# Optimization experiments

Measured on AMD Instinct MI355X. Metric: run time of the kernel, lower is better.

## Reference

```python
import jax, jax.numpy as jnp
import numpy as np

N_NODES = 100000
N_EDGES = 600000
D_IN = 128
D_OUT = 128
N_REL = 16
N_BASES = 8


def setup_inputs() -> dict:
    key = jax.random.key(0)
    ks = jax.random.split(key, 6)
    x = jax.random.normal(ks[0], (N_NODES, D_IN), dtype=jnp.float32)
    edge_index = jax.random.randint(ks[1], (2, N_EDGES), 0, N_NODES, dtype=jnp.int64)
    edge_type = jax.random.randint(ks[2], (N_EDGES,), 0, N_REL, dtype=jnp.int64)
    # xavier-uniform-ish init scales
    b_lim = float(np.sqrt(6.0 / (D_IN + D_OUT)))
    c_lim = float(np.sqrt(6.0 / (N_REL + N_BASES)))
    w_lim = float(np.sqrt(6.0 / (D_IN + D_OUT)))
    bases = jax.random.uniform(ks[3], (N_BASES, D_IN, D_OUT), jnp.float32, -b_lim, b_lim)
    coefficients = jax.random.uniform(ks[4], (N_REL, N_BASES), jnp.float32, -c_lim, c_lim)
    w_self = jax.random.uniform(ks[5], (D_OUT, D_IN), jnp.float32, -w_lim, w_lim)
    return {"x": x, "edge_index": edge_index, "edge_type": edge_type,
            "bases": bases, "coefficients": coefficients, "w_self": w_self}


def reference(x, edge_index, edge_type, bases, coefficients, w_self):
    # self loop: Linear(in, out, bias=False) -> x @ W^T
    out = x @ w_self.T  # [N, D_OUT]
    # relation weights from basis decomposition
    weights = jnp.einsum('rb,bio->rio', coefficients, bases)  # [R, D_IN, D_OUT]
    row, col = edge_index[0], edge_index[1]
    xc = x[col]  # [E, D_IN] gather of source features
    n_rel = weights.shape[0]
    msg = jnp.zeros((xc.shape[0], w_self.shape[0]), dtype=x.dtype)
    # fixed small loop over relations; masked accumulate matches per-relation grouped GEMM
    for r in range(n_rel):
        sel = (edge_type == r)[:, None]
        msg = msg + jnp.where(sel, xc @ weights[r], jnp.zeros((), x.dtype))
    # scatter-add messages to destination rows
    out = out.at[row].add(msg)
    return out
```

## Files before the change

kernel.cpp:

```cpp
#include <hip/hip_runtime.h>

#define NN 100000
#define NE 600000
#define ET (NE + NN)
#define D 128
#define NREL 16
#define SCANB 391

typedef short short8 __attribute__((ext_vector_type(8)));
typedef float f32x4 __attribute__((ext_vector_type(4)));

#define C0 0
#define O0 20
#define CU0 40
#define T0 60

#define WT_OFF 0
#define META_OFF 557056
#define DH_OFF   557568
#define DO_OFF   957568
#define DC_OFF   1357576
#define BS_OFF   1757576
#define SC_OFF   1759168
#define SR_OFF   4559168
#define MP_OFF   7359168
#define MSG_OFF  10159168
#define NEED_A   (MSG_OFF + (size_t)ET * 128 * 2)

__device__ __forceinline__ unsigned short f2bf(float f) {
  unsigned u = __builtin_bit_cast(unsigned, f);
  u += 0x7fffu + ((u >> 16) & 1u);
  return (unsigned short)(u >> 16);
}

__global__ __launch_bounds__(256) void k_weights(const float* __restrict__ bases,
    const float* __restrict__ coef, const float* __restrict__ w_self,
    unsigned short* __restrict__ wT)
{
  int idx = blockIdx.x * 256 + threadIdx.x;
  int r = idx >> 14;
  int t = idx & 16383;
  float v;
  if (r < 16) {
    int o = t >> 7, i = t & 127;
    float acc = 0.f;
    #pragma unroll
    for (int b = 0; b < 8; ++b)
      acc += coef[r * 8 + b] * bases[b * 16384 + i * 128 + o];
    v = acc;
  } else {
    v = w_self[t];
  }
  wT[idx] = f2bf(v);
}

__global__ __launch_bounds__(256) void k_hist(const int* __restrict__ ei,
    const int* __restrict__ et, int* __restrict__ meta, int* __restrict__ dstHist)
{
  __shared__ int h[16];
  int tid = threadIdx.x;
  if (tid < 16) h[tid] = 0;
  __syncthreads();
  for (int e = blockIdx.x * 256 + tid; e < NE; e += gridDim.x * 256) {
    atomicAdd(&h[et[e]], 1);
    atomicAdd(&dstHist[ei[e]], 1);
  }
  __syncthreads();
  if (tid < 16) atomicAdd(&meta[C0 + tid], h[tid]);
}

__global__ __launch_bounds__(256) void k_scan1(const int* __restrict__ dstHist,
    int* __restrict__ dstOff, int* __restrict__ blockSums)
{
  __shared__ int sh[256];
  int tid = threadIdx.x;
  int d = blockIdx.x * 256 + tid;
  int v = (d < NN) ? (dstHist[d] + 1) : 0;
  sh[tid] = v;
  __syncthreads();
  #pragma unroll
  for (int ofs = 1; ofs < 256; ofs <<= 1) {
    int t = (tid >= ofs) ? sh[tid - ofs] : 0;
    __syncthreads();
    sh[tid] += t;
    __syncthreads();
  }
  if (d < NN) dstOff[d] = sh[tid] - v;
  if (tid == 255) blockSums[blockIdx.x] = sh[tid];
}

__global__ __launch_bounds__(512) void k_scan2(int* __restrict__ blockSums, int* __restrict__ meta)
{
  __shared__ int sh[SCANB];
  int tid = threadIdx.x;
  if (tid < SCANB) sh[tid] = blockSums[tid];
  __syncthreads();
  if (tid == 0) {
    int run = 0;
    for (int i = 0; i < SCANB; ++i) { int c = sh[i]; sh[i] = run; run += c; }
    meta[C0 + 16] = NN;
    int off = 0, toff = 0;
    for (int r = 0; r <= 16; ++r) {
      meta[O0 + r] = off;
      meta[CU0 + r] = off;
      meta[T0 + r] = toff;
      int c = meta[C0 + r];
      off += c;
      toff += (c + 63) >> 6;
    }
    meta[O0 + 17] = off;
    meta[T0 + 17] = toff;
  }
  __syncthreads();
  if (tid < SCANB) blockSums[tid] = sh[tid];
}

__global__ __launch_bounds__(256) void k_scan3(int* __restrict__ dstOff,
    const int* __restrict__ blockSums, int* __restrict__ dstCursor)
{
  int tid = threadIdx.x;
  int d = blockIdx.x * 256 + tid;
  int base = blockSums[blockIdx.x];
  if (d < NN) {
    int o = dstOff[d] + base;
    dstOff[d] = o;
    dstCursor[d] = o;
  }
  if (d == NN) dstOff[NN] = ET;
}

__global__ __launch_bounds__(256) void k_self(int* __restrict__ sCol, int* __restrict__ sRow,
    int* __restrict__ mpos, int* __restrict__ dstCursor, int doMsg)
{
  int n = blockIdx.x * 256 + threadIdx.x;
  if (n < NN) {
    sCol[NE + n] = n;
    sRow[NE + n] = n;
    if (doMsg) mpos[NE + n] = atomicAdd(&dstCursor[n], 1);
  }
}

__global__ __launch_bounds__(256) void k_scatter(const int* __restrict__ ei, const int* __restrict__ et,
    int* __restrict__ meta, int* __restrict__ sCol, int* __restrict__ sRow,
    int* __restrict__ mpos, int* __restrict__ dstCursor, int doMsg)
{
  __shared__ int h[16], base[16], lh[16];
  int tid = threadIdx.x;
  int start = blockIdx.x * 4096;
  int end = min(NE, start + 4096);
  if (tid < 16) { h[tid] = 0; lh[tid] = 0; }
  __syncthreads();
  for (int e = start + tid; e < end; e += 256)
    atomicAdd(&h[et[e]], 1);
  __syncthreads();
  if (tid < 16) base[tid] = atomicAdd(&meta[CU0 + tid], h[tid]);
  __syncthreads();
  for (int e = start + tid; e < end; e += 256) {
    int r = et[e];
    int row = ei[e];
    int pos = base[r] + atomicAdd(&lh[r], 1);
    sCol[pos] = ei[NE + e];
    sRow[pos] = row;
    if (doMsg) mpos[pos] = atomicAdd(&dstCursor[row], 1);
  }
}

__global__ __launch_bounds__(256) void k_gemm(const float* __restrict__ x,
    const unsigned short* __restrict__ wT, const int* __restrict__ meta,
    const int* __restrict__ sCol, const int* __restrict__ sRow,
    const int* __restrict__ mpos, unsigned short* __restrict__ msg,
    float* __restrict__ out, int mode)
{
  __shared__ short As[64 * 17 * 8];
  __shared__ int Rows[64];
  __shared__ int Pos[64];
  int b = blockIdx.x;
  if (b >= meta[T0 + 17]) return;
  int r = 0;
  while (r < 16 && meta[T0 + r + 1] <= b) ++r;
  int tile = b - meta[T0 + r];
  int boff = meta[O0 + r];
  int bcnt = meta[C0 + r];
  int e0 = boff + tile * 64;
  int nrows = min(64, boff + bcnt - e0);

  int tid = threadIdx.x;
  int lane = tid & 63, wave = tid >> 6;
  int q = lane >> 4, l15 = lane & 15;

  const unsigned short* wr = wT + r * 16384;
  short8 bf[2][4];
  #pragma unroll
  for (int ns = 0; ns < 2; ++ns) {
    #pragma unroll
    for (int kk = 0; kk < 4; ++kk) {
      int n = wave * 32 + ns * 16 + l15;
      bf[ns][kk] = *(const short8*)(wr + n * 128 + kk * 32 + q * 8);
    }
  }

  int m = tid >> 2, ug = tid & 3;
  bool valid = m < nrows;
  int c = valid ? sCol[e0 + m] : 0;
  const float* xr = x + c * 128;
  #pragma unroll
  for (int s = 0; s < 4; ++s) {
    int u = ug * 4 + s;
    float4 f0 = make_float4(0.f, 0.f, 0.f, 0.f), f1 = f0;
    if (valid) {
      f0 = *(const float4*)(xr + u * 8);
      f1 = *(const float4*)(xr + u * 8 + 4);
    }
    short8 pk;
    pk[0] = (short)f2bf(f0.x); pk[1] = (short)f2bf(f0.y);
    pk[2] = (short)f2bf(f0.z); pk[3] = (short)f2bf(f0.w);
    pk[4] = (short)f2bf(f1.x); pk[5] = (short)f2bf(f1.y);
    pk[6] = (short)f2bf(f1.z); pk[7] = (short)f2bf(f1.w);
    *(short8*)&As[(m * 17 + u) * 8] = pk;
  }
  if (tid < 64) {
    Rows[tid] = (tid < nrows) ? sRow[e0 + tid] : 0;
    Pos[tid] = (mode && tid < nrows) ? mpos[e0 + tid] : 0;
  }
  __syncthreads();

  f32x4 acc[4][2];
  #pragma unroll
  for (int ms = 0; ms < 4; ++ms)
    #pragma unroll
    for (int ns = 0; ns < 2; ++ns)
      acc[ms][ns] = (f32x4){0.f, 0.f, 0.f, 0.f};

  #pragma unroll
  for (int kk = 0; kk < 4; ++kk) {
    short8 af[4];
    #pragma unroll
    for (int ms = 0; ms < 4; ++ms)
      af[ms] = *(const short8*)&As[((ms * 16 + l15) * 17 + kk * 4 + q) * 8];
    #pragma unroll
    for (int ms = 0; ms < 4; ++ms)
      #pragma unroll
      for (int ns = 0; ns < 2; ++ns)
        acc[ms][ns] = __builtin_amdgcn_mfma_f32_16x16x32_bf16(af[ms], bf[ns][kk], acc[ms][ns], 0, 0, 0);
  }

  if (mode) {
    #pragma unroll
    for (int ms = 0; ms < 4; ++ms) {
      #pragma unroll
      for (int reg = 0; reg < 4; ++reg) {
        int mrow = ms * 16 + q * 4 + reg;
        if (mrow < nrows) {
          unsigned short* mp = msg + (size_t)Pos[mrow] * 128 + wave * 32 + l15;
          mp[0]  = f2bf(acc[ms][0][reg]);
          mp[16] = f2bf(acc[ms][1][reg]);
        }
      }
    }
  } else {
    #pragma unroll
    for (int ms = 0; ms < 4; ++ms) {
      #pragma unroll
      for (int reg = 0; reg < 4; ++reg) {
        int mrow = ms * 16 + q * 4 + reg;
        if (mrow < nrows) {
          float* op = out + (size_t)Rows[mrow] * 128 + wave * 32 + l15;
          unsafeAtomicAdd(op, acc[ms][0][reg]);
          unsafeAtomicAdd(op + 16, acc[ms][1][reg]);
        }
      }
    }
  }
}

__global__ __launch_bounds__(256) void k_reduce(const unsigned short* __restrict__ msg,
    const int* __restrict__ dstOff, float* __restrict__ out)
{
  int d = blockIdx.x * 4 + (threadIdx.x >> 6);
  if (d >= NN) return;
  int lane = threadIdx.x & 63;
  int s = dstOff[d], e = dstOff[d + 1];
  float a0 = 0.f, a1 = 0.f;
  const unsigned int* base = (const unsigned int*)msg;
  for (int j = s; j < e; ++j) {
    unsigned int v = base[(size_t)j * 64 + lane];
    a0 += __builtin_bit_cast(float, v << 16);
    a1 += __builtin_bit_cast(float, v & 0xffff0000u);
  }
  float2 w; w.x = a0; w.y = a1;
  *(float2*)(out + (size_t)d * 128 + lane * 2) = w;
}

extern "C" void kernel_launch(void* const* d_in, const int* in_sizes, int n_in,
                              void* d_out, int out_size, void* d_ws, size_t ws_size,
                              hipStream_t stream)
{
  const float* x      = (const float*)d_in[0];
  const int*   ei     = (const int*)d_in[1];
  const int*   et     = (const int*)d_in[2];
  const float* bases  = (const float*)d_in[3];
  const float* coef   = (const float*)d_in[4];
  const float* w_self = (const float*)d_in[5];
  float* out = (float*)d_out;
  char* ws = (char*)d_ws;
  unsigned short* wT = (unsigned short*)(ws + WT_OFF);
  int* meta      = (int*)(ws + META_OFF);
  int* dstHist   = (int*)(ws + DH_OFF);
  int* dstOff    = (int*)(ws + DO_OFF);
  int* dstCursor = (int*)(ws + DC_OFF);
  int* blockSums = (int*)(ws + BS_OFF);
  int* sCol      = (int*)(ws + SC_OFF);
  int* sRow      = (int*)(ws + SR_OFF);
  int* mpos      = (int*)(ws + MP_OFF);
  unsigned short* msg = (unsigned short*)(ws + MSG_OFF);

  const int modeA = (ws_size >= NEED_A) ? 1 : 0;

  hipMemsetAsync(ws + META_OFF, 0, 512 + 400000, stream);
  k_weights<<<(17 * 16384) / 256, 256, 0, stream>>>(bases, coef, w_self, wT);
  k_hist<<<256, 256, 0, stream>>>(ei, et, meta, dstHist);
  if (modeA) {
    k_scan1<<<SCANB, 256, 0, stream>>>(dstHist, dstOff, blockSums);
    k_scan2<<<1, 512, 0, stream>>>(blockSums, meta);
    k_scan3<<<SCANB, 256, 0, stream>>>(dstOff, blockSums, dstCursor);
  } else {
    k_scan2<<<1, 512, 0, stream>>>(blockSums, meta);
    hipMemsetAsync(d_out, 0, (size_t)NN * D * 4, stream);
  }
  k_self<<<SCANB, 256, 0, stream>>>(sCol, sRow, mpos, dstCursor, modeA);
  k_scatter<<<(NE + 4095) / 4096, 256, 0, stream>>>(ei, et, meta, sCol, sRow, mpos, dstCursor, modeA);
  k_gemm<<<10954, 256, 0, stream>>>(x, wT, meta, sCol, sRow, mpos, msg, out, modeA);
  if (modeA)
    k_reduce<<<(NN + 3) / 4, 256, 0, stream>>>(msg, dstOff, out);
}
```

Before: 396.4 us.

## Precast x to bf16, fold self-loop setup into scan, use nontemporal msg traffic

Adds a pre-pass that converts x to bf16 once, so the GEMM gathers half as many bytes per edge row and skips per-tile conversion, at the cost of an extra full pass over x and more workspace. The self-loop index setup moves into k_scan3, which assigns each self-loop the first slot of its destination segment directly instead of using an atomic, and one launch is removed. Message stores and reduce loads become nontemporal, and the reduce loop is unrolled by two with split accumulators for more memory-level parallelism. The bf16 path only runs when the workspace is large enough.

After: 391.5 us. Within noise of the previous version (-1.2%).

```diff
diff --git a/kernel.cpp b/kernel.cpp
--- a/kernel.cpp
+++ b/kernel.cpp
@@ -20,12 +20,15 @@
 #define DH_OFF   557568
 #define DO_OFF   957568
 #define DC_OFF   1357576
-#define BS_OFF   1757576
-#define SC_OFF   1759168
-#define SR_OFF   4559168
-#define MP_OFF   7359168
-#define MSG_OFF  10159168
-#define NEED_A   (MSG_OFF + (size_t)ET * 128 * 2)
+#define BS_OFF   1759168
+#define SC_OFF   1761168
+#define SR_OFF   4561168
+#define MP_OFF   7361168
+#define XB_OFF   10161168
+#define MSGB_OFF 35761168
+#define MSGA_OFF 10161168
+#define NEED_B   (MSGB_OFF + (size_t)ET * 128 * 2)
+#define NEED_A   (MSGA_OFF + (size_t)ET * 128 * 2)
 
 __device__ __forceinline__ unsigned short f2bf(float f) {
   unsigned u = __builtin_bit_cast(unsigned, f);
@@ -52,6 +55,20 @@
     v = w_self[t];
   }
   wT[idx] = f2bf(v);
+}
+
+__global__ __launch_bounds__(256) void k_xcast(const float* __restrict__ x,
+    unsigned short* __restrict__ xb)
+{
+  int i = blockIdx.x * 256 + threadIdx.x;
+  if (i >= NN * D / 4) return;
+  float4 f = *(const float4*)(x + (size_t)i * 4);
+  short8 dummy;
+  unsigned short s0 = f2bf(f.x), s1 = f2bf(f.y), s2 = f2bf(f.z), s3 = f2bf(f.w);
+  (void)dummy;
+  unsigned long long pk = (unsigned long long)s0 | ((unsigned long long)s1 << 16)
+                        | ((unsigned long long)s2 << 32) | ((unsigned long long)s3 << 48);
+  *(unsigned long long*)(xb + (size_t)i * 4) = pk;
 }
 
 __global__ __launch_bounds__(256) void k_hist(const int* __restrict__ ei,
@@ -116,7 +133,8 @@
 }
 
 __global__ __launch_bounds__(256) void k_scan3(int* __restrict__ dstOff,
-    const int* __restrict__ blockSums, int* __restrict__ dstCursor)
+    const int* __restrict__ blockSums, int* __restrict__ dstCursor,
+    int* __restrict__ sCol, int* __restrict__ sRow, int* __restrict__ mpos)
 {
   int tid = threadIdx.x;
   int d = blockIdx.x * 256 + tid;
@@ -124,20 +142,18 @@
   if (d < NN) {
     int o = dstOff[d] + base;
     dstOff[d] = o;
-    dstCursor[d] = o;
+    dstCursor[d] = o + 1;
+    sCol[NE + d] = d;
+    sRow[NE + d] = d;
+    mpos[NE + d] = o;
   }
   if (d == NN) dstOff[NN] = ET;
 }
 
-__global__ __launch_bounds__(256) void k_self(int* __restrict__ sCol, int* __restrict__ sRow,
-    int* __restrict__ mpos, int* __restrict__ dstCursor, int doMsg)
+__global__ __launch_bounds__(256) void k_self0(int* __restrict__ sCol, int* __restrict__ sRow)
 {
   int n = blockIdx.x * 256 + threadIdx.x;
-  if (n < NN) {
-    sCol[NE + n] = n;
-    sRow[NE + n] = n;
-    if (doMsg) mpos[NE + n] = atomicAdd(&dstCursor[n], 1);
-  }
+  if (n < NN) { sCol[NE + n] = n; sRow[NE + n] = n; }
 }
 
 __global__ __launch_bounds__(256) void k_scatter(const int* __restrict__ ei, const int* __restrict__ et,
@@ -165,11 +181,12 @@
   }
 }
 
-__global__ __launch_bounds__(256) void k_gemm(const float* __restrict__ x,
+__global__ __launch_bounds__(256) void k_gemm(const float* __restrict__ xf,
+    const unsigned short* __restrict__ xb,
     const unsigned short* __restrict__ wT, const int* __restrict__ meta,
     const int* __restrict__ sCol, const int* __restrict__ sRow,
     const int* __restrict__ mpos, unsigned short* __restrict__ msg,
-    float* __restrict__ out, int mode)
+    float* __restrict__ out, int xbf, int msgmode)
 {
   __shared__ short As[64 * 17 * 8];
   __shared__ int Rows[64];
@@ -202,25 +219,36 @@
   int m = tid >> 2, ug = tid & 3;
   bool valid = m < nrows;
   int c = valid ? sCol[e0 + m] : 0;
-  const float* xr = x + c * 128;
-  #pragma unroll
-  for (int s = 0; s < 4; ++s) {
-    int u = ug * 4 + s;
-    float4 f0 = make_float4(0.f, 0.f, 0.f, 0.f), f1 = f0;
-    if (valid) {
-      f0 = *(const float4*)(xr + u * 8);
-      f1 = *(const float4*)(xr + u * 8 + 4);
-    }
-    short8 pk;
-    pk[0] = (short)f2bf(f0.x); pk[1] = (short)f2bf(f0.y);
-    pk[2] = (short)f2bf(f0.z); pk[3] = (short)f2bf(f0.w);
-    pk[4] = (short)f2bf(f1.x); pk[5] = (short)f2bf(f1.y);
-    pk[6] = (short)f2bf(f1.z); pk[7] = (short)f2bf(f1.w);
-    *(short8*)&As[(m * 17 + u) * 8] = pk;
+  if (xbf) {
+    const unsigned short* xr = xb + (size_t)c * 128;
+    #pragma unroll
+    for (int s = 0; s < 4; ++s) {
+      int u = ug * 4 + s;
+      short8 pk = (short8)(short)0;
+      if (valid) pk = *(const short8*)(xr + u * 8);
+      *(short8*)&As[(m * 17 + u) * 8] = pk;
+    }
+  } else {
+    const float* xr = xf + (size_t)c * 128;
+    #pragma unroll
+    for (int s = 0; s < 4; ++s) {
+      int u = ug * 4 + s;
+      float4 f0 = make_float4(0.f, 0.f, 0.f, 0.f), f1 = f0;
+      if (valid) {
+        f0 = *(const float4*)(xr + u * 8);
+        f1 = *(const float4*)(xr + u * 8 + 4);
+      }
+      short8 pk;
+      pk[0] = (short)f2bf(f0.x); pk[1] = (short)f2bf(f0.y);
+      pk[2] = (short)f2bf(f0.z); pk[3] = (short)f2bf(f0.w);
+      pk[4] = (short)f2bf(f1.x); pk[5] = (short)f2bf(f1.y);
+      pk[6] = (short)f2bf(f1.z); pk[7] = (short)f2bf(f1.w);
+      *(short8*)&As[(m * 17 + u) * 8] = pk;
+    }
   }
   if (tid < 64) {
     Rows[tid] = (tid < nrows) ? sRow[e0 + tid] : 0;
-    Pos[tid] = (mode && tid < nrows) ? mpos[e0 + tid] : 0;
+    Pos[tid] = (msgmode && tid < nrows) ? mpos[e0 + tid] : 0;
   }
   __syncthreads();
 
@@ -244,7 +272,7 @@
         acc[ms][ns] = __builtin_amdgcn_mfma_f32_16x16x32_bf16(af[ms], bf[ns][kk], acc[ms][ns], 0, 0, 0);
   }
 
-  if (mode) {
+  if (msgmode) {
     #pragma unroll
     for (int ms = 0; ms < 4; ++ms) {
       #pragma unroll
@@ -252,8 +280,8 @@
         int mrow = ms * 16 + q * 4 + reg;
         if (mrow < nrows) {
           unsigned short* mp = msg + (size_t)Pos[mrow] * 128 + wave * 32 + l15;
-          mp[0]  = f2bf(acc[ms][0][reg]);
-          mp[16] = f2bf(acc[ms][1][reg]);
+          __builtin_nontemporal_store(f2bf(acc[ms][0][reg]), mp);
+          __builtin_nontemporal_store(f2bf(acc[ms][1][reg]), mp + 16);
         }
       }
     }
@@ -280,14 +308,23 @@
   if (d >= NN) return;
   int lane = threadIdx.x & 63;
   int s = dstOff[d], e = dstOff[d + 1];
-  float a0 = 0.f, a1 = 0.f;
   const unsigned int* base = (const unsigned int*)msg;
-  for (int j = s; j < e; ++j) {
-    unsigned int v = base[(size_t)j * 64 + lane];
-    a0 += __builtin_bit_cast(float, v << 16);
-    a1 += __builtin_bit_cast(float, v & 0xffff0000u);
-  }
-  float2 w; w.x = a0; w.y = a1;
+  float a0 = 0.f, a1 = 0.f, b0 = 0.f, b1 = 0.f;
+  int j = s;
+  for (; j + 1 < e; j += 2) {
+    unsigned int v0 = __builtin_nontemporal_load(base + (size_t)j * 64 + lane);
+    unsigned int v1 = __builtin_nontemporal_load(base + (size_t)(j + 1) * 64 + lane);
+    a0 += __builtin_bit_cast(float, v0 << 16);
+    a1 += __builtin_bit_cast(float, v0 & 0xffff0000u);
+    b0 += __builtin_bit_cast(float, v1 << 16);
+    b1 += __builtin_bit_cast(float, v1 & 0xffff0000u);
+  }
+  if (j < e) {
+    unsigned int v0 = __builtin_nontemporal_load(base + (size_t)j * 64 + lane);
+    a0 += __builtin_bit_cast(float, v0 << 16);
+    a1 += __builtin_bit_cast(float, v0 & 0xffff0000u);
+  }
+  float2 w; w.x = a0 + b0; w.y = a1 + b1;
   *(float2*)(out + (size_t)d * 128 + lane * 2) = w;
 }
 
@@ -312,24 +349,28 @@
   int* sCol      = (int*)(ws + SC_OFF);
   int* sRow      = (int*)(ws + SR_OFF);
   int* mpos      = (int*)(ws + MP_OFF);
-  unsigned short* msg = (unsigned short*)(ws + MSG_OFF);
-
-  const int modeA = (ws_size >= NEED_A) ? 1 : 0;
+  unsigned short* xb = (unsigned short*)(ws + XB_OFF);
+
+  const int modeB = (ws_size >= NEED_B) ? 1 : 0;
+  const int modeA = (modeB || ws_size >= NEED_A) ? 1 : 0;
+  unsigned short* msg = (unsigned short*)(ws + (modeB ? MSGB_OFF : MSGA_OFF));
 
   hipMemsetAsync(ws + META_OFF, 0, 512 + 400000, stream);
   k_weights<<<(17 * 16384) / 256, 256, 0, stream>>>(bases, coef, w_self, wT);
+  if (modeB)
+    k_xcast<<<(NN * D / 4 + 255) / 256, 256, 0, stream>>>(x, xb);
   k_hist<<<256, 256, 0, stream>>>(ei, et, meta, dstHist);
   if (modeA) {
     k_scan1<<<SCANB, 256, 0, stream>>>(dstHist, dstOff, blockSums);
     k_scan2<<<1, 512, 0, stream>>>(blockSums, meta);
-    k_scan3<<<SCANB, 256, 0, stream>>>(dstOff, blockSums, dstCursor);
+    k_scan3<<<SCANB, 256, 0, stream>>>(dstOff, blockSums, dstCursor, sCol, sRow, mpos);
   } else {
     k_scan2<<<1, 512, 0, stream>>>(blockSums, meta);
+    k_self0<<<SCANB, 256, 0, stream>>>(sCol, sRow);
     hipMemsetAsync(d_out, 0, (size_t)NN * D * 4, stream);
   }
-  k_self<<<SCANB, 256, 0, stream>>>(sCol, sRow, mpos, dstCursor, modeA);
   k_scatter<<<(NE + 4095) / 4096, 256, 0, stream>>>(ei, et, meta, sCol, sRow, mpos, dstCursor, modeA);
-  k_gemm<<<10954, 256, 0, stream>>>(x, wT, meta, sCol, sRow, mpos, msg, out, modeA);
+  k_gemm<<<10954, 256, 0, stream>>>(x, xb, wT, meta, sCol, sRow, mpos, msg, out, modeB, modeA);
   if (modeA)
     k_reduce<<<(NN + 3) / 4, 256, 0, stream>>>(msg, dstOff, out);
 }
```
